# Optimization experiments

Measured on AMD Instinct MI355X. Metric: run time of the kernel, lower is better.

The kernel has to match this reference:

```python
import jax, jax.numpy as jnp
import numpy as np

B, N, D, H = 256, 128, 1024, 4096
PR = 0.2
K1 = int(D * (1 - PR))  # 819 channels kept before net1
K2 = int(H * (1 - PR))  # 3276 channels kept before net2


def setup_inputs() -> dict:
    key = jax.random.key(0)
    ks = jax.random.split(key, 5)
    s = 0.02
    return {
        "x": jax.random.normal(ks[0], (B, N, D), jnp.float32),
        "ws1": jax.random.normal(ks[1], (N,), jnp.float32) * s,  # get_scores1 weight [1,N] -> [N]
        "bs1": jnp.zeros((), jnp.float32),
        "W1": jax.random.normal(ks[2], (H, K1), jnp.float32) * s,  # net1 Linear(K1 -> H)
        "b1": jnp.zeros((H,), jnp.float32),
        "ws2": jax.random.normal(ks[3], (N,), jnp.float32) * s,  # get_scores2 weight
        "bs2": jnp.zeros((), jnp.float32),
        "W2": jax.random.normal(ks[4], (D, K2), jnp.float32) * s,  # net2 Linear(K2 -> D)
        "b2": jnp.zeros((D,), jnp.float32),
    }


def _prune(x, w_s, b_s, k):
    # x: [b, n, c]. Original scores each channel c with Linear(num_patches,1)
    # applied over the patch axis after rearrange to [b, c, n]; equivalent einsum here.
    scores = jnp.einsum('bnc,n->bc', x, w_s) + b_s            # [b, c]
    _, idx = jax.lax.top_k(scores, k)                          # top-k channels per sample
    idx = jnp.sort(idx, axis=-1)                               # boolean-mask gather preserves original channel order
    return jnp.take_along_axis(x, idx[:, None, :], axis=2)    # [b, n, k]


def reference(x, ws1, bs1, W1, b1, ws2, bs2, W2, b2):
    x1 = _prune(x, ws1, bs1, K1)                               # [b, n, K1]
    h = jax.nn.relu(jnp.einsum('bnk,hk->bnh', x1, W1) + b1)    # net1 (dropout=0 eval)
    h2 = _prune(h, ws2, bs2, K2)                               # [b, n, K2]
    return jnp.einsum('bnk,dk->bnd', h2, W2) + b2              # net2
```

## Files before the change

kernel.cpp:

```cpp
#include <hip/hip_runtime.h>
#include <cstdint>
#include <cstddef>

#define B_  256
#define N_  128
#define D_  1024
#define H_  4096
#define K1_ 819
#define K2_ 3276
#define K1P 832
#define K2P 3328
#define KT1 (K1P / 32)
#define KT2D (K2P / 64)
#define LDI1 820
#define LDI2 3280

typedef __bf16 bf16x8 __attribute__((ext_vector_type(8)));
typedef float floatx4 __attribute__((ext_vector_type(4)));
typedef unsigned short ushort4v __attribute__((ext_vector_type(4)));

__device__ __forceinline__ unsigned short f2bf(float f) {
  unsigned u = __float_as_uint(f);
  u += 0x7FFFu + ((u >> 16) & 1u);
  return (unsigned short)(u >> 16);
}
__device__ __forceinline__ float bf2f(unsigned short s) {
  return __uint_as_float(((unsigned)s) << 16);
}

#define GL16(gp, lp) __builtin_amdgcn_global_load_lds( \
    (const __attribute__((address_space(1))) void*)(gp), \
    (__attribute__((address_space(3))) void*)(lp), 16, 0, 0)

__global__ __launch_bounds__(256) void scores1_kernel(const float* __restrict__ x,
                                                      const float* __restrict__ ws1,
                                                      float* __restrict__ scores1) {
  int b = blockIdx.x, t = threadIdx.x;
  __shared__ float w[N_];
  if (t < N_) w[t] = ws1[t];
  __syncthreads();
  const float* xb = x + (size_t)b * N_ * D_;
  double a0 = 0, a1 = 0, a2 = 0, a3 = 0;
  for (int n = 0; n < N_; ++n) {
    double wv = (double)w[n];
    const float* r = xb + (size_t)n * D_ + t;
    a0 += (double)r[0]   * wv;
    a1 += (double)r[256] * wv;
    a2 += (double)r[512] * wv;
    a3 += (double)r[768] * wv;
  }
  float* s = scores1 + (size_t)b * D_ + t;
  s[0]   = (float)a0;
  s[256] = (float)a1;
  s[512] = (float)a2;
  s[768] = (float)a3;
}

__global__ __launch_bounds__(256) void topk_kernel(const float* __restrict__ scores,
                                                   int C, int K, int ldi,
                                                   int* __restrict__ idx_out) {
  int b = blockIdx.x, t = threadIdx.x;
  const int lane = t & 63, wv = t >> 6;
  __shared__ unsigned keys[4096];
  __shared__ unsigned hist[256];
  __shared__ unsigned wsum[4];
  __shared__ unsigned s_sel, s_want;

  for (int c = t; c < C; c += 256) {
    unsigned u = __float_as_uint(scores[(size_t)b * C + c]);
    keys[c] = u ^ ((u & 0x80000000u) ? 0xFFFFFFFFu : 0x80000000u);
  }
  if (t == 0) s_want = (unsigned)K;
  __syncthreads();

  unsigned prefix = 0;
  for (int shift = 24; shift >= 0; shift -= 8) {
    hist[t] = 0u;
    __syncthreads();
    unsigned mask = (shift == 24) ? 0u : (0xFFFFFFFFu << (shift + 8));
    for (int c = t; c < C; c += 256) {
      unsigned k = keys[c];
      if ((k & mask) == (prefix & mask))
        atomicAdd(&hist[(k >> shift) & 0xFFu], 1u);
    }
    __syncthreads();
    if (t == 0) {
      unsigned want = s_want, cum = 0u, sel = 0u;
      for (int d = 255; d >= 0; --d) {
        cum += hist[d];
        if (cum >= want) { sel = (unsigned)d; s_want = want - (cum - hist[d]); break; }
      }
      s_sel = sel;
    }
    __syncthreads();
    prefix |= (s_sel << shift);
  }
  unsigned kth = prefix;
  unsigned n_eq_keep = s_want;
  __syncthreads();

  unsigned base_gt = 0u, base_eq = 0u;
  int nch = C >> 8;
  for (int ch = 0; ch < nch; ++ch) {
    int c = (ch << 8) + t;
    unsigned k = keys[c];
    unsigned gt = (k > kth) ? 1u : 0u;
    unsigned eq = (k == kth) ? 1u : 0u;
    unsigned val = gt | (eq << 16);
    unsigned incl = val;
#pragma unroll
    for (int off = 1; off < 64; off <<= 1) {
      unsigned o = __shfl_up(incl, off, 64);
      if (lane >= off) incl += o;
    }
    if (lane == 63) wsum[wv] = incl;
    __syncthreads();
    unsigned pre = 0u, tot = 0u;
#pragma unroll
    for (int u = 0; u < 4; ++u) {
      unsigned s = wsum[u];
      tot += s;
      if (u < wv) pre += s;
    }
    unsigned excl = incl + pre - val;
    unsigned gt_ex = excl & 0xFFFFu, eq_ex = excl >> 16;
    unsigned eq_before = base_eq + eq_ex;
    bool keep = (gt != 0u) || ((eq != 0u) && (eq_before < n_eq_keep));
    unsigned kept_eq_before = (eq_before < n_eq_keep) ? eq_before : n_eq_keep;
    unsigned pos = base_gt + gt_ex + kept_eq_before;
    if (keep) idx_out[(size_t)b * ldi + pos] = c;
    base_gt += tot & 0xFFFFu;
    base_eq += tot >> 16;
    __syncthreads();
  }
}

__global__ __launch_bounds__(256) void xprep_kernel(const float* __restrict__ x,
                                                    const int* __restrict__ idx1,
                                                    unsigned short* __restrict__ xch,
                                                    unsigned short* __restrict__ xcl) {
  int bn = blockIdx.x;
  int b = bn >> 7;
  const int* idxb = idx1 + (size_t)b * LDI1;
  const float* xr = x + (size_t)bn * D_;
  unsigned short* oh = xch + (size_t)bn * K1P;
  unsigned short* ol = xcl + (size_t)bn * K1P;
  for (int j0 = threadIdx.x * 4; j0 < K1P; j0 += 1024) {
    ushort4v vh, vl;
    if (j0 + 3 < K1_) {
      int4 id = *(const int4*)&idxb[j0];
      float f0 = xr[id.x], f1 = xr[id.y], f2 = xr[id.z], f3 = xr[id.w];
      vh[0] = f2bf(f0); vl[0] = f2bf(f0 - bf2f(vh[0]));
      vh[1] = f2bf(f1); vl[1] = f2bf(f1 - bf2f(vh[1]));
      vh[2] = f2bf(f2); vl[2] = f2bf(f2 - bf2f(vh[2]));
      vh[3] = f2bf(f3); vl[3] = f2bf(f3 - bf2f(vh[3]));
    } else {
#pragma unroll
      for (int e = 0; e < 4; ++e) {
        int j = j0 + e;
        float v = (j < K1_) ? xr[idxb[j]] : 0.f;
        unsigned short hi = f2bf(v);
        vh[e] = hi;
        vl[e] = f2bf(v - bf2f(hi));
      }
    }
    *(ushort4v*)&oh[j0] = vh;
    *(ushort4v*)&ol[j0] = vl;
  }
}

__global__ __launch_bounds__(256) void w1split_kernel(const float* __restrict__ W1,
                                                      unsigned short* __restrict__ w1h,
                                                      unsigned short* __restrict__ w1l) {
  int e = blockIdx.x * 256 + threadIdx.x;
  int k = e % K1P, row = e / K1P;
  float v = (k < K1_) ? W1[(size_t)row * K1_ + k] : 0.f;
  unsigned short hi = f2bf(v);
  unsigned short lo = f2bf(v - bf2f(hi));
  w1h[e] = hi;
  w1l[e] = lo;
}

__global__ __launch_bounds__(256) void w2conv_kernel(const float* __restrict__ W2,
                                                     unsigned short* __restrict__ w2b) {
  int e = blockIdx.x * 256 + threadIdx.x;
  int k = e % K2P, row = e / K2P;
  w2b[e] = (k < K2_) ? f2bf(W2[(size_t)row * K2_ + k]) : (unsigned short)0;
}

__global__ __launch_bounds__(256) void hcompact_kernel(const unsigned short* __restrict__ h,
                                                       const int* __restrict__ idx2,
                                                       unsigned short* __restrict__ hcomp) {
  int bn = blockIdx.x;
  int b = bn >> 7;
  const int* idxb = idx2 + (size_t)b * LDI2;
  const unsigned short* hr = h + (size_t)bn * H_;
  unsigned short* o = hcomp + (size_t)bn * K2P;
  for (int j0 = threadIdx.x * 4; j0 < K2P; j0 += 1024) {
    ushort4v v;
    if (j0 < K2_) {
      int4 id = *(const int4*)&idxb[j0];
      v[0] = hr[id.x]; v[1] = hr[id.y]; v[2] = hr[id.z]; v[3] = hr[id.w];
    } else {
      v[0] = 0; v[1] = 0; v[2] = 0; v[3] = 0;
    }
    *(ushort4v*)&o[j0] = v;
  }
}

#define MF1(d, a, b) d = __builtin_amdgcn_mfma_f32_16x16x32_bf16(a, b, d, 0, 0, 0)

#define CLUSTER24(i0, A0H, A0L, A1H, A1L) \
  __builtin_amdgcn_s_setprio(1); \
  { _Pragma("unroll") \
    for (int j = 0; j < 4; ++j) { \
      MF1(acc[i0][j], A0H, bh[j]); \
      MF1(acc[i0][j], A0H, bl[j]); \
      MF1(acc[i0][j], A0L, bh[j]); \
      MF1(acc[(i0) + 1][j], A1H, bh[j]); \
      MF1(acc[(i0) + 1][j], A1H, bl[j]); \
      MF1(acc[(i0) + 1][j], A1L, bh[j]); \
    } } \
  __builtin_amdgcn_s_setprio(0);

__global__ __launch_bounds__(512, 2) void gemm1_kernel(
    const unsigned short* __restrict__ xch, const unsigned short* __restrict__ xcl,
    const unsigned short* __restrict__ w1h, const unsigned short* __restrict__ w1l,
    const float* __restrict__ b1, const float* __restrict__ ws2,
    unsigned short* __restrict__ h, float* __restrict__ scores2) {
  const int hc0 = blockIdx.x * 256;
  const int b0 = blockIdx.y * 2;
  const int t = threadIdx.x, w = t >> 6, lane = t & 63;
  const int ml = lane & 15, qd = lane >> 4;
  const int wm = w >> 2, wn = w & 3;

  __shared__ unsigned short Ah[2][8192], Al[2][8192], Bh[2][8192], Bl[2][8192];

  floatx4 acc[8][4] = {};

  const unsigned short* Abh = xch + (size_t)b0 * N_ * K1P;
  const unsigned short* Abl = xcl + (size_t)b0 * N_ * K1P;
  const unsigned short* Bbh = w1h + (size_t)hc0 * K1P;
  const unsigned short* Bbl = w1l + (size_t)hc0 * K1P;

  const int c0 = w * 64 + lane, c1 = c0 + 512;
  const size_t off0 = (size_t)(((c0 >> 6) << 4) | (c0 & 15)) * K1P + (size_t)(((c0 >> 4) & 3) * 8);
  const size_t off1 = (size_t)(((c1 >> 6) << 4) | (c1 & 15)) * K1P + (size_t)(((c1 >> 4) & 3) * 8);
  const int lb0 = (w * 64) * 8;
  const int lb1 = (512 + w * 64) * 8;

  auto aof = [&](int i) { return ((wm * 8 + i) * 64 + qd * 16 + ml) * 8; };

  GL16(Abh + off0, &Ah[0][lb0]); GL16(Abh + off1, &Ah[0][lb1]);
  GL16(Abl + off0, &Al[0][lb0]); GL16(Abl + off1, &Al[0][lb1]);
  GL16(Bbh + off0, &Bh[0][lb0]); GL16(Bbh + off1, &Bh[0][lb1]);
  GL16(Bbl + off0, &Bl[0][lb0]); GL16(Bbl + off1, &Bl[0][lb1]);

  for (int kt = 0; kt < KT1; ++kt) {
    const int cur = kt & 1, nxt = cur ^ 1;
    const size_t kk = (size_t)(kt + 1) * 32;
    const bool stg = (kt + 1 < KT1);

    if (stg) { GL16(Bbh + off0 + kk, &Bh[nxt][lb0]); GL16(Bbh + off1 + kk, &Bh[nxt][lb1]); }
    if (stg) asm volatile("s_waitcnt vmcnt(2)" ::: "memory");
    else     asm volatile("s_waitcnt vmcnt(0)" ::: "memory");
    __builtin_amdgcn_s_barrier();

    bf16x8 bh[4], bl[4];
#pragma unroll
    for (int j = 0; j < 4; ++j) {
      const int bo = ((wn * 4 + j) * 64 + qd * 16 + ml) * 8;
      bh[j] = *(const bf16x8*)&Bh[cur][bo];
      bl[j] = *(const bf16x8*)&Bl[cur][bo];
    }
    bf16x8 a0h = *(const bf16x8*)&Ah[cur][aof(0)];
    bf16x8 a0l = *(const bf16x8*)&Al[cur][aof(0)];
    bf16x8 a1h = *(const bf16x8*)&Ah[cur][aof(1)];
    bf16x8 a1l = *(const bf16x8*)&Al[cur][aof(1)];
    bf16x8 a2h = *(const bf16x8*)&Ah[cur][aof(2)];
    bf16x8 a2l = *(const bf16x8*)&Al[cur][aof(2)];
    bf16x8 a3h = *(const bf16x8*)&Ah[cur][aof(3)];
    bf16x8 a3l = *(const bf16x8*)&Al[cur][aof(3)];
    if (stg) { GL16(Bbl + off0 + kk, &Bl[nxt][lb0]); GL16(Bbl + off1 + kk, &Bl[nxt][lb1]); }
    __builtin_amdgcn_sched_barrier(0);
    CLUSTER24(0, a0h, a0l, a1h, a1l)
    __builtin_amdgcn_s_barrier();

    bf16x8 a4h = *(const bf16x8*)&Ah[cur][aof(4)];
    bf16x8 a4l = *(const bf16x8*)&Al[cur][aof(4)];
    bf16x8 a5h = *(const bf16x8*)&Ah[cur][aof(5)];
    bf16x8 a5l = *(const bf16x8*)&Al[cur][aof(5)];
    if (stg) { GL16(Abh + off0 + kk, &Ah[nxt][lb0]); GL16(Abh + off1 + kk, &Ah[nxt][lb1]); }
    __builtin_amdgcn_sched_barrier(0);
    CLUSTER24(2, a2h, a2l, a3h, a3l)
    __builtin_amdgcn_s_barrier();

    bf16x8 a6h = *(const bf16x8*)&Ah[cur][aof(6)];
    bf16x8 a6l = *(const bf16x8*)&Al[cur][aof(6)];
    bf16x8 a7h = *(const bf16x8*)&Ah[cur][aof(7)];
    bf16x8 a7l = *(const bf16x8*)&Al[cur][aof(7)];
    if (stg) { GL16(Abl + off0 + kk, &Al[nxt][lb0]); GL16(Abl + off1 + kk, &Al[nxt][lb1]); }
    __builtin_amdgcn_sched_barrier(0);
    CLUSTER24(4, a4h, a4l, a5h, a5l)
    __builtin_amdgcn_s_barrier();

    __builtin_amdgcn_sched_barrier(0);
    CLUSTER24(6, a6h, a6l, a7h, a7l)
    __builtin_amdgcn_s_barrier();
  }

  const int bb = b0 + wm;
  float bias[4];
#pragma unroll
  for (int j = 0; j < 4; ++j) bias[j] = b1[hc0 + wn * 64 + j * 16 + ml];
  float sc[4] = {0.f, 0.f, 0.f, 0.f};
#pragma unroll
  for (int i = 0; i < 8; ++i) {
#pragma unroll
    for (int r = 0; r < 4; ++r) {
      const int n = i * 16 + qd * 4 + r;
      const float wsn = ws2[n];
      unsigned short* hp = h + ((size_t)(bb * N_ + n)) * H_ + hc0 + wn * 64;
#pragma unroll
      for (int j = 0; j < 4; ++j) {
        float v = acc[i][j][r] + bias[j];
        v = fmaxf(v, 0.f);
        hp[j * 16 + ml] = f2bf(v);
        sc[j] += v * wsn;
      }
    }
  }
#pragma unroll
  for (int j = 0; j < 4; ++j) {
    sc[j] += __shfl_xor(sc[j], 16);
    sc[j] += __shfl_xor(sc[j], 32);
  }
  if (lane < 16) {
#pragma unroll
    for (int j = 0; j < 4; ++j)
      scores2[(size_t)bb * H_ + hc0 + wn * 64 + j * 16 + lane] = sc[j];
  }
}

#define MF2(d, a, b) d = __builtin_amdgcn_mfma_f32_16x16x32_bf16(a, b, d, 0, 0, 0)

#define CL16(i0, A0, A1, A2r, A3, BB) \
  __builtin_amdgcn_s_setprio(1); \
  { _Pragma("unroll") \
    for (int j = 0; j < 4; ++j) { \
      MF2(acc[(i0)][j], A0, BB[j]); \
      MF2(acc[(i0) + 1][j], A1, BB[j]); \
      MF2(acc[(i0) + 2][j], A2r, BB[j]); \
      MF2(acc[(i0) + 3][j], A3, BB[j]); \
    } } \
  __builtin_amdgcn_s_setprio(0);

__global__ __launch_bounds__(512, 2) void gemm2_kernel(
    const unsigned short* __restrict__ hcomp, const unsigned short* __restrict__ w2b,
    const float* __restrict__ b2, float* __restrict__ out) {
  const int d0 = blockIdx.x * 256;
  const int b0 = blockIdx.y * 2;
  const int t = threadIdx.x, w = t >> 6, lane = t & 63;
  const int ml = lane & 15, qd = lane >> 4;
  const int wm = w >> 2, wn = w & 3;

  __shared__ unsigned short As[2][2][8192], Bs[2][2][8192];

  floatx4 acc[8][4] = {};

  const unsigned short* Ab = hcomp + (size_t)b0 * N_ * K2P;
  const unsigned short* Bb = w2b + (size_t)d0 * K2P;

  const int c0 = w * 64 + lane, c1 = c0 + 512;
  const size_t off0 = (size_t)(((c0 >> 6) << 4) | (c0 & 15)) * K2P + (size_t)(((c0 >> 4) & 3) * 8);
  const size_t off1 = (size_t)(((c1 >> 6) << 4) | (c1 & 15)) * K2P + (size_t)(((c1 >> 4) & 3) * 8);
  const int lb0 = (w * 64) * 8, lb1 = (512 + w * 64) * 8;

  auto aof = [&](int i) { return ((wm * 8 + i) * 64 + qd * 16 + ml) * 8; };
  auto bof = [&](int j) { return ((wn * 4 + j) * 64 + qd * 16 + ml) * 8; };

  GL16(Ab + off0,      &As[0][0][lb0]); GL16(Ab + off1,      &As[0][0][lb1]);
  GL16(Ab + off0 + 32, &As[0][1][lb0]); GL16(Ab + off1 + 32, &As[0][1][lb1]);
  GL16(Bb + off0,      &Bs[0][0][lb0]); GL16(Bb + off1,      &Bs[0][0][lb1]);
  GL16(Bb + off0 + 32, &Bs[0][1][lb0]); GL16(Bb + off1 + 32, &Bs[0][1][lb1]);

  for (int kt = 0; kt < KT2D; ++kt) {
    const int cur = kt & 1, nxt = cur ^ 1;
    const size_t kk = (size_t)(kt + 1) * 64;
    const bool stg = (kt + 1 < KT2D);

    if (stg) { GL16(Ab + off0 + kk, &As[nxt][0][lb0]); GL16(Ab + off1 + kk, &As[nxt][0][lb1]); }
    if (stg) asm volatile("s_waitcnt vmcnt(2)" ::: "memory");
    else     asm volatile("s_waitcnt vmcnt(0)" ::: "memory");
    __builtin_amdgcn_s_barrier();

    bf16x8 bh0[4];
#pragma unroll
    for (int j = 0; j < 4; ++j) bh0[j] = *(const bf16x8*)&Bs[cur][0][bof(j)];
    bf16x8 a0 = *(const bf16x8*)&As[cur][0][aof(0)];
    bf16x8 a1 = *(const bf16x8*)&As[cur][0][aof(1)];
    bf16x8 a2 = *(const bf16x8*)&As[cur][0][aof(2)];
    bf16x8 a3 = *(const bf16x8*)&As[cur][0][aof(3)];
    bf16x8 a4 = *(const bf16x8*)&As[cur][0][aof(4)];
    bf16x8 a5 = *(const bf16x8*)&As[cur][0][aof(5)];
    bf16x8 a6 = *(const bf16x8*)&As[cur][0][aof(6)];
    bf16x8 a7 = *(const bf16x8*)&As[cur][0][aof(7)];
    if (stg) { GL16(Ab + off0 + kk + 32, &As[nxt][1][lb0]); GL16(Ab + off1 + kk + 32, &As[nxt][1][lb1]); }
    __builtin_amdgcn_sched_barrier(0);
    CL16(0, a0, a1, a2, a3, bh0)
    __builtin_amdgcn_s_barrier();

    bf16x8 bh1[4];
#pragma unroll
    for (int j = 0; j < 4; ++j) bh1[j] = *(const bf16x8*)&Bs[cur][1][bof(j)];
    bf16x8 e0 = *(const bf16x8*)&As[cur][1][aof(0)];
    bf16x8 e1 = *(const bf16x8*)&As[cur][1][aof(1)];
    bf16x8 e2 = *(const bf16x8*)&As[cur][1][aof(2)];
    bf16x8 e3 = *(const bf16x8*)&As[cur][1][aof(3)];
    if (stg) { GL16(Bb + off0 + kk, &Bs[nxt][0][lb0]); GL16(Bb + off1 + kk, &Bs[nxt][0][lb1]); }
    __builtin_amdgcn_sched_barrier(0);
    CL16(4, a4, a5, a6, a7, bh0)
    __builtin_amdgcn_s_barrier();

    bf16x8 e4 = *(const bf16x8*)&As[cur][1][aof(4)];
    bf16x8 e5 = *(const bf16x8*)&As[cur][1][aof(5)];
    bf16x8 e6 = *(const bf16x8*)&As[cur][1][aof(6)];
    bf16x8 e7 = *(const bf16x8*)&As[cur][1][aof(7)];
    if (stg) { GL16(Bb + off0 + kk + 32, &Bs[nxt][1][lb0]); GL16(Bb + off1 + kk + 32, &Bs[nxt][1][lb1]); }
    __builtin_amdgcn_sched_barrier(0);
    CL16(0, e0, e1, e2, e3, bh1)
    __builtin_amdgcn_s_barrier();

    __builtin_amdgcn_sched_barrier(0);
    CL16(4, e4, e5, e6, e7, bh1)
    __builtin_amdgcn_s_barrier();
  }

  const int bb = b0 + wm;
  float bias[4];
#pragma unroll
  for (int j = 0; j < 4; ++j) bias[j] = b2[d0 + wn * 64 + j * 16 + ml];
#pragma unroll
  for (int i = 0; i < 8; ++i) {
#pragma unroll
    for (int r = 0; r < 4; ++r) {
      const int n = i * 16 + qd * 4 + r;
      float* op = out + ((size_t)(bb * N_ + n)) * D_ + d0 + wn * 64;
#pragma unroll
      for (int j = 0; j < 4; ++j)
        op[j * 16 + ml] = acc[i][j][r] + bias[j];
    }
  }
}

extern "C" void kernel_launch(void* const* d_in, const int* in_sizes, int n_in,
                              void* d_out, int out_size, void* d_ws, size_t ws_size,
                              hipStream_t stream) {
  (void)in_sizes; (void)n_in; (void)out_size; (void)ws_size;
  const float* x   = (const float*)d_in[0];
  const float* ws1 = (const float*)d_in[1];
  const float* W1  = (const float*)d_in[3];
  const float* b1  = (const float*)d_in[4];
  const float* ws2 = (const float*)d_in[5];
  const float* W2  = (const float*)d_in[7];
  const float* b2  = (const float*)d_in[8];
  float* out = (float*)d_out;

  char* p = (char*)d_ws;
  auto alloc = [&](size_t bytes) {
    char* r = p;
    p += (bytes + 255) & ~(size_t)255;
    return r;
  };
  float* scores1 = (float*)alloc((size_t)B_ * D_ * sizeof(float));
  int*   idx1    = (int*)  alloc((size_t)B_ * LDI1 * sizeof(int));
  float* scores2 = (float*)alloc((size_t)B_ * H_ * sizeof(float));
  int*   idx2    = (int*)  alloc((size_t)B_ * LDI2 * sizeof(int));
  unsigned short* w1h = (unsigned short*)alloc((size_t)H_ * K1P * sizeof(short));
  unsigned short* w1l = (unsigned short*)alloc((size_t)H_ * K1P * sizeof(short));
  unsigned short* w2b = (unsigned short*)alloc((size_t)D_ * K2P * sizeof(short));
  unsigned short* h   = (unsigned short*)alloc((size_t)B_ * N_ * H_ * sizeof(short));
  size_t xc_bytes    = (size_t)B_ * N_ * K1P * sizeof(short);
  size_t hcomp_bytes = (size_t)B_ * N_ * K2P * sizeof(short);
  char* region = alloc(hcomp_bytes > 2 * xc_bytes ? hcomp_bytes : 2 * xc_bytes);
  unsigned short* xch   = (unsigned short*)region;
  unsigned short* xcl   = (unsigned short*)(region + xc_bytes);
  unsigned short* hcomp = (unsigned short*)region;

  scores1_kernel<<<B_, 256, 0, stream>>>(x, ws1, scores1);
  topk_kernel<<<B_, 256, 0, stream>>>(scores1, D_, K1_, LDI1, idx1);
  xprep_kernel<<<B_ * N_, 256, 0, stream>>>(x, idx1, xch, xcl);
  w1split_kernel<<<(H_ * K1P) / 256, 256, 0, stream>>>(W1, w1h, w1l);
  w2conv_kernel<<<(D_ * K2P) / 256, 256, 0, stream>>>(W2, w2b);
  gemm1_kernel<<<dim3(H_ / 256, B_ / 2), 512, 0, stream>>>(xch, xcl, w1h, w1l, b1, ws2, h, scores2);
  topk_kernel<<<B_, 256, 0, stream>>>(scores2, H_, K2_, LDI2, idx2);
  hcompact_kernel<<<B_ * N_, 256, 0, stream>>>(h, idx2, hcomp);
  gemm2_kernel<<<dim3(D_ / 256, B_ / 2), 512, 0, stream>>>(hcomp, w2b, b2, out);
}
```

Baseline: 1.437 ms.

## Widen scores1 blocks, parallelize top-k bucket scan, reorder MFMA cluster

The scores1 kernel now runs 1024 threads per block, one output channel per thread, instead of 256 threads each handling four channels. This raises parallelism for the double-precision reduction. The top-k radix select replaces the serial single-thread 256-bin suffix scan with a wave-shuffle parallel scan across all threads. The gemm1 MFMA cluster is reordered so that consecutive MFMAs write independent accumulators, which reduces back-to-back dependency stalls.

```diff
diff --git a/kernel.cpp b/kernel.cpp
--- a/kernel.cpp
+++ b/kernel.cpp
@@ -32,28 +32,18 @@
     (const __attribute__((address_space(1))) void*)(gp), \
     (__attribute__((address_space(3))) void*)(lp), 16, 0, 0)
 
-__global__ __launch_bounds__(256) void scores1_kernel(const float* __restrict__ x,
-                                                      const float* __restrict__ ws1,
-                                                      float* __restrict__ scores1) {
+__global__ __launch_bounds__(1024) void scores1_kernel(const float* __restrict__ x,
+                                                       const float* __restrict__ ws1,
+                                                       float* __restrict__ scores1) {
   int b = blockIdx.x, t = threadIdx.x;
   __shared__ float w[N_];
   if (t < N_) w[t] = ws1[t];
   __syncthreads();
-  const float* xb = x + (size_t)b * N_ * D_;
-  double a0 = 0, a1 = 0, a2 = 0, a3 = 0;
-  for (int n = 0; n < N_; ++n) {
-    double wv = (double)w[n];
-    const float* r = xb + (size_t)n * D_ + t;
-    a0 += (double)r[0]   * wv;
-    a1 += (double)r[256] * wv;
-    a2 += (double)r[512] * wv;
-    a3 += (double)r[768] * wv;
-  }
-  float* s = scores1 + (size_t)b * D_ + t;
-  s[0]   = (float)a0;
-  s[256] = (float)a1;
-  s[512] = (float)a2;
-  s[768] = (float)a3;
+  const float* xb = x + (size_t)b * N_ * D_ + t;
+  double a = 0;
+  for (int n = 0; n < N_; ++n)
+    a += (double)xb[(size_t)n * D_] * (double)w[n];
+  scores1[(size_t)b * D_ + t] = (float)a;
 }
 
 __global__ __launch_bounds__(256) void topk_kernel(const float* __restrict__ scores,
@@ -84,13 +74,24 @@
         atomicAdd(&hist[(k >> shift) & 0xFFu], 1u);
     }
     __syncthreads();
-    if (t == 0) {
-      unsigned want = s_want, cum = 0u, sel = 0u;
-      for (int d = 255; d >= 0; --d) {
-        cum += hist[d];
-        if (cum >= want) { sel = (unsigned)d; s_want = want - (cum - hist[d]); break; }
-      }
-      s_sel = sel;
+    const unsigned want = s_want;
+    const unsigned hv = hist[255 - t];
+    unsigned incl = hv;
+#pragma unroll
+    for (int off = 1; off < 64; off <<= 1) {
+      unsigned o = __shfl_up(incl, off, 64);
+      if (lane >= off) incl += o;
+    }
+    if (lane == 63) wsum[wv] = incl;
+    __syncthreads();
+    unsigned pre = 0u;
+#pragma unroll
+    for (int u = 0; u < 4; ++u)
+      if (u < wv) pre += wsum[u];
+    const unsigned suf = incl + pre;
+    if (suf >= want && (suf - hv) < want) {
+      s_sel = (unsigned)(255 - t);
+      s_want = want - (suf - hv);
     }
     __syncthreads();
     prefix |= (s_sel << shift);
@@ -213,14 +214,18 @@
 #define CLUSTER24(i0, A0H, A0L, A1H, A1L) \
   __builtin_amdgcn_s_setprio(1); \
   { _Pragma("unroll") \
-    for (int j = 0; j < 4; ++j) { \
-      MF1(acc[i0][j], A0H, bh[j]); \
-      MF1(acc[i0][j], A0H, bl[j]); \
-      MF1(acc[i0][j], A0L, bh[j]); \
-      MF1(acc[(i0) + 1][j], A1H, bh[j]); \
-      MF1(acc[(i0) + 1][j], A1H, bl[j]); \
-      MF1(acc[(i0) + 1][j], A1L, bh[j]); \
-    } } \
+    for (int j = 0; j < 4; ++j) MF1(acc[i0][j], A0H, bh[j]); \
+    _Pragma("unroll") \
+    for (int j = 0; j < 4; ++j) MF1(acc[(i0) + 1][j], A1H, bh[j]); \
+    _Pragma("unroll") \
+    for (int j = 0; j < 4; ++j) MF1(acc[i0][j], A0H, bl[j]); \
+    _Pragma("unroll") \
+    for (int j = 0; j < 4; ++j) MF1(acc[(i0) + 1][j], A1H, bl[j]); \
+    _Pragma("unroll") \
+    for (int j = 0; j < 4; ++j) MF1(acc[i0][j], A0L, bh[j]); \
+    _Pragma("unroll") \
+    for (int j = 0; j < 4; ++j) MF1(acc[(i0) + 1][j], A1L, bh[j]); \
+  } \
   __builtin_amdgcn_s_setprio(0);
 
 __global__ __launch_bounds__(512, 2) void gemm1_kernel(
@@ -487,7 +492,7 @@
   unsigned short* xcl   = (unsigned short*)(region + xc_bytes);
   unsigned short* hcomp = (unsigned short*)region;
 
-  scores1_kernel<<<B_, 256, 0, stream>>>(x, ws1, scores1);
+  scores1_kernel<<<B_, 1024, 0, stream>>>(x, ws1, scores1);
   topk_kernel<<<B_, 256, 0, stream>>>(scores1, D_, K1_, LDI1, idx1);
   xprep_kernel<<<B_ * N_, 256, 0, stream>>>(x, idx1, xch, xcl);
   w1split_kernel<<<(H_ * K1P) / 256, 256, 0, stream>>>(W1, w1h, w1l);
```

After: 1.362 ms. 1.05x faster.
